# Performance work log

Hardware: AMD Instinct MI355X
Metric: run time of the kernel (lower is better)

## Reference

```python
import jax, jax.numpy as jnp
import numpy as np

POS_W, NEG_W = 2.0, 40.0
MARGIN, THRESH = 0.1, 0.5


def setup_inputs() -> dict:
    key = jax.random.key(0)
    k1, k2 = jax.random.split(key)
    B, D, C = 4096, 128, 100
    batch = jax.random.normal(k1, (B, D), dtype=jnp.float32)
    # metric-learning embeddings are L2-normalized -> sim in [-1, 1]
    batch = batch / jnp.linalg.norm(batch, axis=1, keepdims=True)
    labels = jax.random.randint(k2, (B,), 0, C)
    return {"batch": batch, "labels": labels}


def reference(batch, labels):
    B = batch.shape[0]
    sim = batch @ batch.T  # [B, B]
    eq = labels[:, None] == labels[None, :]
    not_self = ~jnp.eye(B, dtype=bool)
    pos_mask = eq & not_self   # positives, excluding anchor itself
    neg_mask = ~eq             # negatives

    # per-row hardest thresholds (masked min/max)
    min_pos = jnp.min(jnp.where(pos_mask, sim, jnp.inf), axis=1)   # [B]
    max_neg = jnp.max(jnp.where(neg_mask, sim, -jnp.inf), axis=1)  # [B]

    neg_keep = neg_mask & (sim + MARGIN > min_pos[:, None])
    pos_keep = pos_mask & (sim - MARGIN < max_neg[:, None])

    # masked exponentials: exp(-inf) = 0 keeps it overflow-safe
    pos_sum = jnp.sum(jnp.exp(jnp.where(pos_keep, -POS_W * (sim - THRESH), -jnp.inf)), axis=1)
    neg_sum = jnp.sum(jnp.exp(jnp.where(neg_keep, NEG_W * (sim - THRESH), -jnp.inf)), axis=1)

    row_loss = jnp.log1p(pos_sum) / POS_W + jnp.log1p(neg_sum) / NEG_W  # [B]

    # original skips rows where either kept-set is empty
    valid = jnp.any(pos_keep, axis=1) & jnp.any(neg_keep, axis=1)
    n_valid = jnp.maximum(jnp.sum(valid), 1)
    return jnp.sum(jnp.where(valid, row_loss, 0.0)) / n_valid
```

## Files before the change

### kernel.cpp

```cpp
#include <hip/hip_runtime.h>
#include <math.h>

#define Bsz 4096
#define Dk 128
#define RPB 16
#define NBLK (Bsz / RPB)
#define THREADS 1024
#define NW 16
#define CPW (Bsz / NW)
#define CT (CPW / 16)

typedef __attribute__((ext_vector_type(8))) short short8;
typedef __attribute__((ext_vector_type(4))) float f32x4;

__device__ __forceinline__ unsigned short f2bf(float f) {
  unsigned u = __float_as_uint(f);
  u = (u + 0x7fffu + ((u >> 16) & 1u)) >> 16;
  return (unsigned short)u;
}

__global__ __launch_bounds__(256)
void convert_kernel(const float* __restrict__ X, short* __restrict__ Xt) {
  int i = blockIdx.x * 256 + threadIdx.x;
  int col = i >> 4, kb = i & 15;
  const float4* q = (const float4*)(X + col * Dk + kb * 8);
  float4 v0 = q[0], v1 = q[1];
  short8 r;
  r[0] = (short)f2bf(v0.x); r[1] = (short)f2bf(v0.y);
  r[2] = (short)f2bf(v0.z); r[3] = (short)f2bf(v0.w);
  r[4] = (short)f2bf(v1.x); r[5] = (short)f2bf(v1.y);
  r[6] = (short)f2bf(v1.z); r[7] = (short)f2bf(v1.w);
  *(short8*)(Xt + (size_t)(kb * Bsz + col) * 8) = r;
}

__device__ __forceinline__ short8 ldfrag(const short* __restrict__ Xt, int col, int ks, int lg) {
  return *(const short8*)(Xt + (size_t)(((ks << 2) + lg) * Bsz + col) * 8);
}

__global__ __launch_bounds__(THREADS, 4)
void mono(const short* __restrict__ Xt, const int* __restrict__ labels,
          float* __restrict__ row_loss, float* __restrict__ row_valid) {
  const int tid = threadIdx.x;
  const int w  = tid >> 6;
  const int l  = tid & 63;
  const int lg = l >> 4;
  const int lr = l & 15;
  const int r0 = blockIdx.x * RPB;

  __shared__ float red[2][NW][RPB];
  __shared__ float thp_s[RPB], thn_s[RPB], vld_s[RPB];

  short8 afrag[4];
  for (int ks = 0; ks < 4; ++ks) afrag[ks] = ldfrag(Xt, r0 + lr, ks, lg);
  int labr[4];
  for (int rg = 0; rg < 4; ++rg) labr[rg] = labels[r0 + lg * 4 + rg];

  float mnp[4], mxn[4];
  for (int rg = 0; rg < 4; ++rg) { mnp[rg] = INFINITY; mxn[rg] = -INFINITY; }

  for (int ct = 0; ct < CT; ++ct) {
    const int ctc  = w * CPW + ct * 16;
    const int colv = ctc + lr;
    short8 bfrag[4];
    for (int ks = 0; ks < 4; ++ks) bfrag[ks] = ldfrag(Xt, colv, ks, lg);
    const int labc = labels[colv];

    f32x4 acc = {0.f, 0.f, 0.f, 0.f};
    for (int ks = 0; ks < 4; ++ks)
      acc = __builtin_amdgcn_mfma_f32_16x16x32_bf16(afrag[ks], bfrag[ks], acc, 0, 0, 0);
    const bool diag = (ctc == r0);
    for (int rg = 0; rg < 4; ++rg) {
      float s    = acc[rg];
      bool  eq   = (labc == labr[rg]);
      bool  self = diag && (lr == lg * 4 + rg);
      if (eq && !self) mnp[rg] = fminf(mnp[rg], s);
      if (!eq)         mxn[rg] = fmaxf(mxn[rg], s);
    }
  }
  for (int rg = 0; rg < 4; ++rg) {
    for (int m = 1; m < 16; m <<= 1) {
      mnp[rg] = fminf(mnp[rg], __shfl_xor(mnp[rg], m, 64));
      mxn[rg] = fmaxf(mxn[rg], __shfl_xor(mxn[rg], m, 64));
    }
  }
  if (lr == 0)
    for (int rg = 0; rg < 4; ++rg) {
      red[0][w][lg * 4 + rg] = mnp[rg];
      red[1][w][lg * 4 + rg] = mxn[rg];
    }
  __syncthreads();

  if (tid < RPB) {
    float a = INFINITY, b = -INFINITY;
    for (int ww = 0; ww < NW; ++ww) {
      a = fminf(a, red[0][ww][tid]);
      b = fmaxf(b, red[1][ww][tid]);
    }
    thp_s[tid] = b + 0.1f;
    thn_s[tid] = a - 0.1f;
    vld_s[tid] = (a - 0.1f < b) ? 1.f : 0.f;
  }
  __syncthreads();

  float tp[4], tn[4];
  for (int rg = 0; rg < 4; ++rg) {
    tp[rg] = thp_s[lg * 4 + rg];
    tn[rg] = thn_s[lg * 4 + rg];
  }
  float ap[4] = {0.f, 0.f, 0.f, 0.f}, an[4] = {0.f, 0.f, 0.f, 0.f};

  for (int ct = 0; ct < CT; ++ct) {
    const int ctc  = w * CPW + ct * 16;
    const int colv = ctc + lr;
    short8 bfrag[4];
    for (int ks = 0; ks < 4; ++ks) bfrag[ks] = ldfrag(Xt, colv, ks, lg);
    const int labc = labels[colv];

    f32x4 acc = {0.f, 0.f, 0.f, 0.f};
    for (int ks = 0; ks < 4; ++ks)
      acc = __builtin_amdgcn_mfma_f32_16x16x32_bf16(afrag[ks], bfrag[ks], acc, 0, 0, 0);
    const bool diag = (ctc == r0);
    for (int rg = 0; rg < 4; ++rg) {
      float s    = acc[rg];
      bool  eq   = (labc == labr[rg]);
      bool  self = diag && (lr == lg * 4 + rg);
      bool  kp   = eq && !self && (s < tp[rg]);
      bool  kn   = (!eq) && (s > tn[rg]);
      float argp = fmaf(s, -2.885390082f, 1.442695041f);
      float argn = fmaf(s, 57.70780163f, -28.85390082f);
      float e = exp2f(kp ? argp : argn);
      ap[rg] += kp ? e : 0.f;
      an[rg] += kn ? e : 0.f;
    }
  }
  for (int rg = 0; rg < 4; ++rg) {
    for (int m = 1; m < 16; m <<= 1) {
      ap[rg] += __shfl_xor(ap[rg], m, 64);
      an[rg] += __shfl_xor(an[rg], m, 64);
    }
  }
  __syncthreads();
  if (lr == 0)
    for (int rg = 0; rg < 4; ++rg) {
      red[0][w][lg * 4 + rg] = ap[rg];
      red[1][w][lg * 4 + rg] = an[rg];
    }
  __syncthreads();

  if (tid < RPB) {
    float P = 0.f, N = 0.f;
    for (int ww = 0; ww < NW; ++ww) { P += red[0][ww][tid]; N += red[1][ww][tid]; }
    bool v = vld_s[tid] > 0.f;
    row_loss[r0 + tid]  = v ? (log1pf(P) * 0.5f + log1pf(N) * 0.025f) : 0.f;
    row_valid[r0 + tid] = v ? 1.f : 0.f;
  }
}

__global__ __launch_bounds__(1024)
void finalize(const float* __restrict__ row_loss, const float* __restrict__ row_valid,
              float* __restrict__ out) {
  int tid = threadIdx.x;
  float s = 0.f, c = 0.f;
  for (int r = tid; r < Bsz; r += 1024) {
    s += row_loss[r];
    c += row_valid[r];
  }
  for (int m = 1; m < 64; m <<= 1) {
    s += __shfl_xor(s, m, 64);
    c += __shfl_xor(c, m, 64);
  }
  __shared__ float rs[16], rc[16];
  int w = tid >> 6, lz = tid & 63;
  if (lz == 0) { rs[w] = s; rc[w] = c; }
  __syncthreads();
  if (tid == 0) {
    float ts = 0.f, tc = 0.f;
    for (int i = 0; i < 16; ++i) { ts += rs[i]; tc += rc[i]; }
    out[0] = ts / fmaxf(tc, 1.0f);
  }
}

extern "C" void kernel_launch(void* const* d_in, const int* in_sizes, int n_in,
                              void* d_out, int out_size, void* d_ws, size_t ws_size,
                              hipStream_t stream) {
  const float* X      = (const float*)d_in[0];
  const int*   labels = (const int*)d_in[1];

  char* ws = (char*)d_ws;
  short* Xt        = (short*)ws;
  float* row_loss  = (float*)(ws + 1048576);
  float* row_valid = (float*)(ws + 1048576 + 16384);

  convert_kernel<<<256, 256, 0, stream>>>(X, Xt);
  mono<<<NBLK, THREADS, 0, stream>>>(Xt, labels, row_loss, row_valid);
  finalize<<<1, 1024, 0, stream>>>(row_loss, row_valid, (float*)d_out);
}
```

Before: 38.58 us.

## Cache fp16-encoded similarities in registers to skip recomputing GEMM in second pass

The first pass now stores each similarity, encoded with label-equality and self flags as offsets, into packed fp16 registers. The second pass decodes these instead of reloading B fragments and labels and recomputing MFMAs. This removes half of the global loads and matrix work, at the cost of more registers and reduced precision in the cached similarities.

```diff
diff --git a/kernel.cpp b/kernel.cpp
--- a/kernel.cpp
+++ b/kernel.cpp
@@ -12,6 +12,7 @@
 
 typedef __attribute__((ext_vector_type(8))) short short8;
 typedef __attribute__((ext_vector_type(4))) float f32x4;
+typedef _Float16 h2 __attribute__((ext_vector_type(2)));
 
 __device__ __forceinline__ unsigned short f2bf(float f) {
   unsigned u = __float_as_uint(f);
@@ -55,9 +56,11 @@
   int labr[4];
   for (int rg = 0; rg < 4; ++rg) labr[rg] = labels[r0 + lg * 4 + rg];
 
+  h2 sims[2 * CT];
   float mnp[4], mxn[4];
   for (int rg = 0; rg < 4; ++rg) { mnp[rg] = INFINITY; mxn[rg] = -INFINITY; }
 
+#pragma unroll
   for (int ct = 0; ct < CT; ++ct) {
     const int ctc  = w * CPW + ct * 16;
     const int colv = ctc + lr;
@@ -69,14 +72,23 @@
     for (int ks = 0; ks < 4; ++ks)
       acc = __builtin_amdgcn_mfma_f32_16x16x32_bf16(afrag[ks], bfrag[ks], acc, 0, 0, 0);
     const bool diag = (ctc == r0);
+    float enc[4];
+#pragma unroll
     for (int rg = 0; rg < 4; ++rg) {
       float s    = acc[rg];
       bool  eq   = (labc == labr[rg]);
       bool  self = diag && (lr == lg * 4 + rg);
       if (eq && !self) mnp[rg] = fminf(mnp[rg], s);
       if (!eq)         mxn[rg] = fmaxf(mxn[rg], s);
-    }
-  }
+      float e = eq ? s + 4.0f : s;
+      enc[rg] = self ? 8.0f : e;
+    }
+    h2 p0; p0[0] = (_Float16)enc[0]; p0[1] = (_Float16)enc[1];
+    h2 p1; p1[0] = (_Float16)enc[2]; p1[1] = (_Float16)enc[3];
+    sims[2 * ct]     = p0;
+    sims[2 * ct + 1] = p1;
+  }
+
   for (int rg = 0; rg < 4; ++rg) {
     for (int m = 1; m < 16; m <<= 1) {
       mnp[rg] = fminf(mnp[rg], __shfl_xor(mnp[rg], m, 64));
@@ -109,23 +121,15 @@
   }
   float ap[4] = {0.f, 0.f, 0.f, 0.f}, an[4] = {0.f, 0.f, 0.f, 0.f};
 
+#pragma unroll
   for (int ct = 0; ct < CT; ++ct) {
-    const int ctc  = w * CPW + ct * 16;
-    const int colv = ctc + lr;
-    short8 bfrag[4];
-    for (int ks = 0; ks < 4; ++ks) bfrag[ks] = ldfrag(Xt, colv, ks, lg);
-    const int labc = labels[colv];
-
-    f32x4 acc = {0.f, 0.f, 0.f, 0.f};
-    for (int ks = 0; ks < 4; ++ks)
-      acc = __builtin_amdgcn_mfma_f32_16x16x32_bf16(afrag[ks], bfrag[ks], acc, 0, 0, 0);
-    const bool diag = (ctc == r0);
-    for (int rg = 0; rg < 4; ++rg) {
-      float s    = acc[rg];
-      bool  eq   = (labc == labr[rg]);
-      bool  self = diag && (lr == lg * 4 + rg);
-      bool  kp   = eq && !self && (s < tp[rg]);
-      bool  kn   = (!eq) && (s > tn[rg]);
+#pragma unroll
+    for (int rg = 0; rg < 4; ++rg) {
+      float v  = (float)sims[2 * ct + (rg >> 1)][rg & 1];
+      bool  eq = v > 2.0f;
+      float s  = eq ? v - 4.0f : v;
+      bool  kp = eq && (s < tp[rg]);
+      bool  kn = (!eq) && (s > tn[rg]);
       float argp = fmaf(s, -2.885390082f, 1.442695041f);
       float argn = fmaf(s, 57.70780163f, -28.85390082f);
       float e = exp2f(kp ? argp : argn);
```

Measured after the change: 38.83 us. Within noise of the previous version (+0.6%).
